# Optimization experiments

Hardware: AMD Instinct MI355X
Metric: run time of the kernel (lower is better)

## Reference

```python
import jax, jax.numpy as jnp
import numpy as np

HIDDEN = 4096
N_HEADS = 32
N_KV_HEADS = 8
HEAD_DIM = 128
ROPE_THETA = 10000.0
B, S = 2, 2048


def _rope_cos_sin(seq_len, head_dim, theta):
    inv_freq = 1.0 / (theta ** (jnp.arange(0, head_dim, 2, dtype=jnp.float32) / head_dim))
    t = jnp.arange(seq_len, dtype=jnp.float32)
    freqs = jnp.einsum('i,j->ij', t, inv_freq)          # [S, D/2]
    emb = jnp.concatenate([freqs, freqs], axis=-1)      # [S, D]
    return jnp.cos(emb), jnp.sin(emb)


def _rotate_half(x):
    x1, x2 = x[..., : x.shape[-1] // 2], x[..., x.shape[-1] // 2 :]
    return jnp.concatenate([-x2, x1], axis=-1)


def setup_inputs() -> dict:
    key = jax.random.key(0)
    k0, k1, k2, k3, k4 = jax.random.split(key, 5)
    scale = 0.02
    return {
        'hidden_states': jax.random.normal(k0, (B, S, HIDDEN), dtype=jnp.float32),
        'wq': jax.random.normal(k1, (N_HEADS * HEAD_DIM, HIDDEN), dtype=jnp.float32) * scale,
        'wk': jax.random.normal(k2, (N_KV_HEADS * HEAD_DIM, HIDDEN), dtype=jnp.float32) * scale,
        'wv': jax.random.normal(k3, (N_KV_HEADS * HEAD_DIM, HIDDEN), dtype=jnp.float32) * scale,
        'wo': jax.random.normal(k4, (HIDDEN, N_HEADS * HEAD_DIM), dtype=jnp.float32) * scale,
    }


def reference(hidden_states, wq, wk, wv, wo):
    bsz, q_len, _ = hidden_states.shape
    n_rep = N_HEADS // N_KV_HEADS

    # Q/K/V projections (nn.Linear: x @ W.T), reshape to [B, H, S, D]
    q = (hidden_states @ wq.T).reshape(bsz, q_len, N_HEADS, HEAD_DIM).transpose(0, 2, 1, 3)
    k = (hidden_states @ wk.T).reshape(bsz, q_len, N_KV_HEADS, HEAD_DIM).transpose(0, 2, 1, 3)
    v = (hidden_states @ wv.T).reshape(bsz, q_len, N_KV_HEADS, HEAD_DIM).transpose(0, 2, 1, 3)

    # RoPE (position_ids = arange) broadcast over heads: cos/sin [1,1,S,D]
    cos, sin = _rope_cos_sin(q_len, HEAD_DIM, ROPE_THETA)
    cos = cos[None, None]
    sin = sin[None, None]
    q = q * cos + _rotate_half(q) * sin
    k = k * cos + _rotate_half(k) * sin

    # repeat_kv: [B, KVH, S, D] -> [B, H, S, D]
    k = jnp.repeat(k, n_rep, axis=1)
    v = jnp.repeat(v, n_rep, axis=1)

    # scaled dot-product attention with causal mask
    scores = jnp.einsum('bhqd,bhkd->bhqk', q, k) / jnp.sqrt(jnp.float32(HEAD_DIM))
    causal = jnp.tril(jnp.ones((q_len, q_len), dtype=bool))
    scores = jnp.where(causal[None, None], scores, jnp.finfo(scores.dtype).min)
    probs = jax.nn.softmax(scores.astype(jnp.float32), axis=-1).astype(q.dtype)
    attn = jnp.einsum('bhqk,bhkd->bhqd', probs, v)

    # merge heads and output projection
    attn = attn.transpose(0, 2, 1, 3).reshape(bsz, q_len, N_HEADS * HEAD_DIM)
    return attn @ wo.T
```

## Files before the change

kernel.cpp:

```cpp
#include <hip/hip_runtime.h>
#include <hip/hip_bf16.h>

typedef __attribute__((ext_vector_type(8))) __bf16 bf16x8;
typedef __attribute__((ext_vector_type(4))) float f32x4;

#define SEQ 2048
#define BATCH 2
#define LDQ 6144

__device__ __forceinline__ void stc(float* p, float v)          { *p = v; }
__device__ __forceinline__ void stc(__hip_bfloat16* p, float v) { *p = __float2bfloat16(v); }

__device__ __forceinline__ void async_copy16(const __hip_bfloat16* g, __hip_bfloat16* lds) {
    __builtin_amdgcn_global_load_lds(
        (const __attribute__((address_space(1))) unsigned int*)g,
        (__attribute__((address_space(3))) unsigned int*)lds,
        16, 0, 0);
}

__global__ void f2b_kernel(const float* __restrict__ s, __hip_bfloat16* __restrict__ d, int n8)
{
    const int i = blockIdx.x * blockDim.x + threadIdx.x;
    if (i >= n8) return;
    const float4 a = ((const float4*)s)[i * 2];
    const float4 b = ((const float4*)s)[i * 2 + 1];
    __hip_bfloat16 t[8];
    t[0] = __float2bfloat16(a.x); t[1] = __float2bfloat16(a.y);
    t[2] = __float2bfloat16(a.z); t[3] = __float2bfloat16(a.w);
    t[4] = __float2bfloat16(b.x); t[5] = __float2bfloat16(b.y);
    t[6] = __float2bfloat16(b.z); t[7] = __float2bfloat16(b.w);
    ((uint4*)d)[i] = *(const uint4*)t;
}

template<typename TC>
__global__ __launch_bounds__(512, 2) void gemm256_kernel(
    const __hip_bfloat16* __restrict__ A,
    const __hip_bfloat16* __restrict__ B,
    TC* __restrict__ C,
    int M, int N, int K)
{
    __shared__ __align__(16) __hip_bfloat16 sAB[2][2][2][256][32];
    const int NT = K >> 6;

    const int tid  = threadIdx.x;
    const int wave = tid >> 6;
    const int lane = tid & 63;
    const int quad = lane >> 4;
    const int l16  = lane & 15;
    const int wm = wave >> 2;
    const int wn = wave & 3;

    const int nbm = M >> 8;
    const int nwg = nbm * (N >> 8);
    int wg = blockIdx.x;
    {
        const int q8 = nwg >> 3, r8 = nwg & 7;
        const int xcd = wg & 7, base = wg >> 3;
        wg = (xcd < r8 ? xcd * (q8 + 1) : r8 * (q8 + 1) + (xcd - r8) * q8) + base;
    }
    const int m0 = (wg % nbm) << 8;
    const int n0 = (wg / nbm) << 8;

    const int srow = lane >> 2;
    const int scol = ((lane & 3) ^ ((lane >> 3) & 3)) * 8;
    const int qsw  = (quad ^ ((l16 >> 1) & 3)) * 8;

    auto stage = [&](int tile, int matr, int kh) {
        const __hip_bfloat16* g = matr ? B : A;
        const int b0 = matr ? n0 : m0;
        const int buf = tile & 1;
        #pragma unroll
        for (int j = 0; j < 2; ++j) {
            const int c = wave * 2 + j;
            async_copy16(g + (size_t)(b0 + c * 16 + srow) * K + tile * 64 + kh * 32 + scol,
                         &sAB[buf][matr][kh][c * 16][0]);
        }
    };

    stage(0, 0, 0); stage(0, 1, 0); stage(0, 0, 1); stage(0, 1, 1);
    stage(1, 0, 0); stage(1, 1, 0);
    asm volatile("s_waitcnt vmcnt(8)" ::: "memory");
    __builtin_amdgcn_s_barrier();

    f32x4 acc[8][4] = {};
    bf16x8 bv[4];

    for (int T = 0; T < NT; ++T) {
        const int buf = T & 1;
        #pragma unroll
        for (int q = 0; q < 4; ++q) {
            const int kh = q >> 1;
            const int rh = (q == 1 || q == 2) ? 1 : 0;

            bf16x8 av[4];
            #pragma unroll
            for (int i = 0; i < 4; ++i)
                av[i] = *(const bf16x8*)&sAB[buf][0][kh][wm * 128 + (rh * 4 + i) * 16 + l16][qsw];
            if (q == 0 || q == 2) {
                #pragma unroll
                for (int j = 0; j < 4; ++j)
                    bv[j] = *(const bf16x8*)&sAB[buf][1][kh][wn * 64 + j * 16 + l16][qsw];
            }

            if (q == 0) { if (T + 1 < NT) stage(T + 1, 0, 1); }
            if (q == 1) { if (T + 1 < NT) stage(T + 1, 1, 1); }
            if (q == 2) { if (T + 2 < NT) stage(T + 2, 0, 0); }
            if (q == 3) { if (T + 2 < NT) stage(T + 2, 1, 0); }

            __builtin_amdgcn_s_barrier();
            asm volatile("s_waitcnt lgkmcnt(0)" ::: "memory");
            __builtin_amdgcn_s_setprio(1);
            #pragma unroll
            for (int i = 0; i < 4; ++i)
                #pragma unroll
                for (int j = 0; j < 4; ++j)
                    acc[rh * 4 + i][j] = __builtin_amdgcn_mfma_f32_16x16x32_bf16(
                        av[i], bv[j], acc[rh * 4 + i][j], 0, 0, 0);
            __builtin_amdgcn_s_setprio(0);

            if (q == 1) {
                if (T < NT - 1)       asm volatile("s_waitcnt vmcnt(8)" ::: "memory");
                else                  asm volatile("s_waitcnt vmcnt(0)" ::: "memory");
            }
            if (q == 3) {
                if (T < NT - 2)       asm volatile("s_waitcnt vmcnt(8)" ::: "memory");
                else if (T == NT - 2) asm volatile("s_waitcnt vmcnt(4)" ::: "memory");
            }
            __builtin_amdgcn_s_barrier();
        }
    }

    #pragma unroll
    for (int i = 0; i < 8; ++i)
        #pragma unroll
        for (int j = 0; j < 4; ++j)
            #pragma unroll
            for (int r = 0; r < 4; ++r) {
                const int m = m0 + wm * 128 + i * 16 + quad * 4 + r;
                const int n = n0 + wn * 64 + j * 16 + l16;
                stc(&C[(size_t)m * N + n], acc[i][j][r]);
            }
}

__global__ void rope_kernel(__hip_bfloat16* __restrict__ X, int rows, int n_heads,
                            int ld, int col0)
{
    const int idx = blockIdx.x * blockDim.x + threadIdx.x;
    const int total = rows * n_heads * 64;
    if (idx >= total) return;
    const int j   = idx & 63;
    const int h   = (idx >> 6) % n_heads;
    const int row = idx / (n_heads * 64);
    const int s   = row & (SEQ - 1);

    const float invf = expf(-(float)j * (9.210340371976184f / 64.0f));
    const float ang = (float)s * invf;
    const float c = cosf(ang), sn = sinf(ang);

    const size_t base = (size_t)row * ld + col0 + h * 128;
    const float x1 = __bfloat162float(X[base + j]);
    const float x2 = __bfloat162float(X[base + 64 + j]);
    X[base + j]      = __float2bfloat16(x1 * c - x2 * sn);
    X[base + 64 + j] = __float2bfloat16(x2 * c + x1 * sn);
}

__global__ __launch_bounds__(256) void vtrans_kernel(
    const __hip_bfloat16* __restrict__ V, __hip_bfloat16* __restrict__ VT)
{
    __shared__ unsigned int T[64][65];

    const int tid = threadIdx.x;
    const int n0 = blockIdx.x * 64;
    const int s0 = blockIdx.y * 64;
    const int b  = blockIdx.z;

    #pragma unroll
    for (int it = 0; it < 2; it++) {
        const int idx = it * 256 + tid;
        const int sr = idx >> 3, nc = (idx & 7) * 8;
        const uint4 v = *(const uint4*)(V + (size_t)(b * SEQ + s0 + sr) * LDQ + n0 + nc);
        const unsigned short* u = (const unsigned short*)&v;
        #pragma unroll
        for (int i = 0; i < 8; i++) T[sr][nc + i] = u[i];
    }
    __syncthreads();
    #pragma unroll
    for (int it = 0; it < 2; it++) {
        const int idx = it * 256 + tid;
        const int nn = idx >> 3, sc = (idx & 7) * 8;
        unsigned short u[8];
        #pragma unroll
        for (int i = 0; i < 8; i++) u[i] = (unsigned short)T[sc + i][nn];
        *(uint4*)(VT + (size_t)(b * 1024 + n0 + nn) * SEQ + s0 + sc) = *(const uint4*)u;
    }
}

__global__ __launch_bounds__(64) void attn_kernel(
    const __hip_bfloat16* __restrict__ QKV,
    const __hip_bfloat16* __restrict__ VT,
    __hip_bfloat16* __restrict__ O)
{
    __shared__ __align__(16) __hip_bfloat16 Pw[2][16][72];

    const int lane = threadIdx.x;
    const int quad = lane >> 4;
    const int l16  = lane & 15;
    const int h   = blockIdx.y;
    const int b   = blockIdx.z;
    const int kvh = h >> 2;

    bf16x8 ones;
    {
        __hip_bfloat16 t[8];
        for (int i = 0; i < 8; i++) t[i] = __float2bfloat16(1.0f);
        ones = *(const bf16x8*)t;
    }

    const __hip_bfloat16* Kbase = QKV + (size_t)b * SEQ * LDQ + 4096 + kvh * 128 + quad * 8;
    const __hip_bfloat16* Vbase = VT + (size_t)(b * 1024 + kvh * 128) * SEQ + quad * 8;
    const float scale = 0.08838834764831845f;
    const float shift = 12.0f;

    for (int ph = 0; ph < 2; ph++) {
        const int qt = ph ? blockIdx.x : 63 - blockIdx.x;
        const int q0 = qt * 32;

        bf16x8 aq[2][4];
        for (int ch = 0; ch < 2; ch++)
            for (int c = 0; c < 4; c++)
                aq[ch][c] = *(const bf16x8*)(QKV + (size_t)(b * SEQ + q0 + ch * 16 + l16) * LDQ
                                                 + h * 128 + c * 32 + quad * 8);

        f32x4 o[2][8] = {};
        f32x4 lsum[2] = {};

        const int nt = qt / 2 + 1;
        for (int kt = 0; kt < nt; kt++) {
            f32x4 sc[2][4] = {};
            #pragma unroll
            for (int g = 0; g < 4; g++) {
                const __hip_bfloat16* kr = Kbase + (size_t)(kt * 64 + g * 16 + l16) * LDQ;
                bf16x8 bk[4];
                #pragma unroll
                for (int c = 0; c < 4; c++) bk[c] = *(const bf16x8*)(kr + c * 32);
                #pragma unroll
                for (int c = 0; c < 4; c++) {
                    sc[0][g] = __builtin_amdgcn_mfma_f32_16x16x32_bf16(aq[0][c], bk[c], sc[0][g], 0, 0, 0);
                    sc[1][g] = __builtin_amdgcn_mfma_f32_16x16x32_bf16(aq[1][c], bk[c], sc[1][g], 0, 0, 0);
                }
            }

            const bool diag = (kt == nt - 1);
            #pragma unroll
            for (int ch = 0; ch < 2; ch++)
                #pragma unroll
                for (int rr = 0; rr < 4; rr++) {
                    float s[4];
                    #pragma unroll
                    for (int g = 0; g < 4; g++) s[g] = sc[ch][g][rr] * scale - shift;
                    if (diag) {
                        const int qg = q0 + ch * 16 + quad * 4 + rr;
                        #pragma unroll
                        for (int g = 0; g < 4; g++)
                            if (kt * 64 + g * 16 + l16 > qg) s[g] = -1e30f;
                    }
                    #pragma unroll
                    for (int g = 0; g < 4; g++)
                        Pw[ch][quad * 4 + rr][g * 16 + l16] = __float2bfloat16(__expf(s[g]));
                }
            asm volatile("s_waitcnt lgkmcnt(0)" ::: "memory");

            bf16x8 ap[2][2];
            #pragma unroll
            for (int ch = 0; ch < 2; ch++) {
                ap[ch][0] = *(const bf16x8*)(&Pw[ch][l16][quad * 8]);
                ap[ch][1] = *(const bf16x8*)(&Pw[ch][l16][32 + quad * 8]);
                lsum[ch] = __builtin_amdgcn_mfma_f32_16x16x32_bf16(ap[ch][0], ones, lsum[ch], 0, 0, 0);
                lsum[ch] = __builtin_amdgcn_mfma_f32_16x16x32_bf16(ap[ch][1], ones, lsum[ch], 0, 0, 0);
            }

            #pragma unroll
            for (int nc = 0; nc < 8; nc++) {
                const __hip_bfloat16* vr = Vbase + (size_t)(nc * 16 + l16) * SEQ + kt * 64;
                const bf16x8 bv0 = *(const bf16x8*)(vr);
                const bf16x8 bv1 = *(const bf16x8*)(vr + 32);
                o[0][nc] = __builtin_amdgcn_mfma_f32_16x16x32_bf16(ap[0][0], bv0, o[0][nc], 0, 0, 0);
                o[0][nc] = __builtin_amdgcn_mfma_f32_16x16x32_bf16(ap[0][1], bv1, o[0][nc], 0, 0, 0);
                o[1][nc] = __builtin_amdgcn_mfma_f32_16x16x32_bf16(ap[1][0], bv0, o[1][nc], 0, 0, 0);
                o[1][nc] = __builtin_amdgcn_mfma_f32_16x16x32_bf16(ap[1][1], bv1, o[1][nc], 0, 0, 0);
            }
        }

        for (int ch = 0; ch < 2; ch++)
            for (int rr = 0; rr < 4; rr++) {
                const float inv = 1.0f / lsum[ch][rr];
                const size_t row = (size_t)(b * SEQ + q0 + ch * 16 + quad * 4 + rr);
                for (int nc = 0; nc < 8; nc++)
                    O[row * 4096 + h * 128 + nc * 16 + l16] = __float2bfloat16(o[ch][nc][rr] * inv);
            }
    }
}

extern "C" void kernel_launch(void* const* d_in, const int* in_sizes, int n_in,
                              void* d_out, int out_size, void* d_ws, size_t ws_size,
                              hipStream_t stream)
{
    const float* X  = (const float*)d_in[0];
    const float* Wq = (const float*)d_in[1];
    const float* Wk = (const float*)d_in[2];
    const float* Wv = (const float*)d_in[3];
    const float* Wo = (const float*)d_in[4];
    float* out = (float*)d_out;

    const size_t MB = 1048576;
    char* ws = (char*)d_ws;
    __hip_bfloat16* Xb   = (__hip_bfloat16*)(ws);
    __hip_bfloat16* WB   = (__hip_bfloat16*)(ws + 32 * MB);
    __hip_bfloat16* Wkb  = (__hip_bfloat16*)(ws + 64 * MB);
    __hip_bfloat16* Wvb  = (__hip_bfloat16*)(ws + 72 * MB);
    __hip_bfloat16* QKVb = (__hip_bfloat16*)(ws + 80 * MB);
    __hip_bfloat16* Ab   = Xb;
    __hip_bfloat16* Wob  = WB;
    __hip_bfloat16* VT   = Wkb;

    const int M = BATCH * SEQ;

    f2b_kernel<<<(M * 4096 / 8 + 255) / 256, 256, 0, stream>>>(X,  Xb,  M * 4096 / 8);
    f2b_kernel<<<(4096 * 4096 / 8 + 255) / 256, 256, 0, stream>>>(Wq, WB,  4096 * 4096 / 8);
    f2b_kernel<<<(1024 * 4096 / 8 + 255) / 256, 256, 0, stream>>>(Wk, Wkb, 1024 * 4096 / 8);
    f2b_kernel<<<(1024 * 4096 / 8 + 255) / 256, 256, 0, stream>>>(Wv, Wvb, 1024 * 4096 / 8);

    gemm256_kernel<__hip_bfloat16>
        <<<dim3((M / 256) * (LDQ / 256)), 512, 0, stream>>>(Xb, WB, QKVb, M, LDQ, 4096);

    f2b_kernel<<<(4096 * 4096 / 8 + 255) / 256, 256, 0, stream>>>(Wo, Wob, 4096 * 4096 / 8);

    rope_kernel<<<(M * 32 * 64 + 255) / 256, 256, 0, stream>>>(QKVb, M, 32, LDQ, 0);
    rope_kernel<<<(M * 8 * 64 + 255) / 256, 256, 0, stream>>>(QKVb, M, 8, LDQ, 4096);

    vtrans_kernel<<<dim3(16, SEQ / 64, BATCH), 256, 0, stream>>>(QKVb + 5120, VT);

    attn_kernel<<<dim3(32, 32, BATCH), 64, 0, stream>>>(QKVb, VT, Ab);

    gemm256_kernel<float>
        <<<dim3((M / 256) * (4096 / 256)), 512, 0, stream>>>(Ab, Wob, out, M, 4096, 4096);
}
```

Baseline: 844.6 us.

## Split attention query tile across two waves per block

The attention kernel now launches 128 threads per block, with each wave handling one 16-row query chunk instead of one wave handling both chunks. This halves per-wave register use for accumulators and doubles the number of waves in flight, to hide global-load latency of K/V. The cost is that each wave loads K and V tiles separately, so global and cache traffic for K/V roughly doubles. No sync is needed because each wave has its own Pw slice.

```diff
diff --git a/kernel.cpp b/kernel.cpp
--- a/kernel.cpp
+++ b/kernel.cpp
@@ -195,14 +195,15 @@
     }
 }
 
-__global__ __launch_bounds__(64) void attn_kernel(
+__global__ __launch_bounds__(128, 4) void attn_kernel(
     const __hip_bfloat16* __restrict__ QKV,
     const __hip_bfloat16* __restrict__ VT,
     __hip_bfloat16* __restrict__ O)
 {
     __shared__ __align__(16) __hip_bfloat16 Pw[2][16][72];
 
-    const int lane = threadIdx.x;
+    const int wv   = threadIdx.x >> 6;
+    const int lane = threadIdx.x & 63;
     const int quad = lane >> 4;
     const int l16  = lane & 15;
     const int h   = blockIdx.y;
@@ -225,18 +226,17 @@
         const int qt = ph ? blockIdx.x : 63 - blockIdx.x;
         const int q0 = qt * 32;
 
-        bf16x8 aq[2][4];
-        for (int ch = 0; ch < 2; ch++)
-            for (int c = 0; c < 4; c++)
-                aq[ch][c] = *(const bf16x8*)(QKV + (size_t)(b * SEQ + q0 + ch * 16 + l16) * LDQ
-                                                 + h * 128 + c * 32 + quad * 8);
-
-        f32x4 o[2][8] = {};
-        f32x4 lsum[2] = {};
+        bf16x8 aq[4];
+        for (int c = 0; c < 4; c++)
+            aq[c] = *(const bf16x8*)(QKV + (size_t)(b * SEQ + q0 + wv * 16 + l16) * LDQ
+                                         + h * 128 + c * 32 + quad * 8);
+
+        f32x4 o[8] = {};
+        f32x4 lsum = {};
 
         const int nt = qt / 2 + 1;
         for (int kt = 0; kt < nt; kt++) {
-            f32x4 sc[2][4] = {};
+            f32x4 sc[4] = {};
             #pragma unroll
             for (int g = 0; g < 4; g++) {
                 const __hip_bfloat16* kr = Kbase + (size_t)(kt * 64 + g * 16 + l16) * LDQ;
@@ -244,60 +244,50 @@
                 #pragma unroll
                 for (int c = 0; c < 4; c++) bk[c] = *(const bf16x8*)(kr + c * 32);
                 #pragma unroll
-                for (int c = 0; c < 4; c++) {
-                    sc[0][g] = __builtin_amdgcn_mfma_f32_16x16x32_bf16(aq[0][c], bk[c], sc[0][g], 0, 0, 0);
-                    sc[1][g] = __builtin_amdgcn_mfma_f32_16x16x32_bf16(aq[1][c], bk[c], sc[1][g], 0, 0, 0);
-                }
+                for (int c = 0; c < 4; c++)
+                    sc[g] = __builtin_amdgcn_mfma_f32_16x16x32_bf16(aq[c], bk[c], sc[g], 0, 0, 0);
             }
 
             const bool diag = (kt == nt - 1);
             #pragma unroll
-            for (int ch = 0; ch < 2; ch++)
-                #pragma unroll
-                for (int rr = 0; rr < 4; rr++) {
-                    float s[4];
-                    #pragma unroll
-                    for (int g = 0; g < 4; g++) s[g] = sc[ch][g][rr] * scale - shift;
-                    if (diag) {
-                        const int qg = q0 + ch * 16 + quad * 4 + rr;
-                        #pragma unroll
-                        for (int g = 0; g < 4; g++)
-                            if (kt * 64 + g * 16 + l16 > qg) s[g] = -1e30f;
-                    }
+            for (int rr = 0; rr < 4; rr++) {
+                float s[4];
+                #pragma unroll
+                for (int g = 0; g < 4; g++) s[g] = sc[g][rr] * scale - shift;
+                if (diag) {
+                    const int qg = q0 + wv * 16 + quad * 4 + rr;
                     #pragma unroll
                     for (int g = 0; g < 4; g++)
-                        Pw[ch][quad * 4 + rr][g * 16 + l16] = __float2bfloat16(__expf(s[g]));
+                        if (kt * 64 + g * 16 + l16 > qg) s[g] = -1e30f;
                 }
+                #pragma unroll
+                for (int g = 0; g < 4; g++)
+                    Pw[wv][quad * 4 + rr][g * 16 + l16] = __float2bfloat16(__expf(s[g]));
+            }
             asm volatile("s_waitcnt lgkmcnt(0)" ::: "memory");
 
-            bf16x8 ap[2][2];
-            #pragma unroll
-            for (int ch = 0; ch < 2; ch++) {
-                ap[ch][0] = *(const bf16x8*)(&Pw[ch][l16][quad * 8]);
-                ap[ch][1] = *(const bf16x8*)(&Pw[ch][l16][32 + quad * 8]);
-                lsum[ch] = __builtin_amdgcn_mfma_f32_16x16x32_bf16(ap[ch][0], ones, lsum[ch], 0, 0, 0);
-                lsum[ch] = __builtin_amdgcn_mfma_f32_16x16x32_bf16(ap[ch][1], ones, lsum[ch], 0, 0, 0);
-            }
+            bf16x8 ap[2];
+            ap[0] = *(const bf16x8*)(&Pw[wv][l16][quad * 8]);
+            ap[1] = *(const bf16x8*)(&Pw[wv][l16][32 + quad * 8]);
+            lsum = __builtin_amdgcn_mfma_f32_16x16x32_bf16(ap[0], ones, lsum, 0, 0, 0);
+            lsum = __builtin_amdgcn_mfma_f32_16x16x32_bf16(ap[1], ones, lsum, 0, 0, 0);
 
             #pragma unroll
             for (int nc = 0; nc < 8; nc++) {
                 const __hip_bfloat16* vr = Vbase + (size_t)(nc * 16 + l16) * SEQ + kt * 64;
                 const bf16x8 bv0 = *(const bf16x8*)(vr);
                 const bf16x8 bv1 = *(const bf16x8*)(vr + 32);
-                o[0][nc] = __builtin_amdgcn_mfma_f32_16x16x32_bf16(ap[0][0], bv0, o[0][nc], 0, 0, 0);
-                o[0][nc] = __builtin_amdgcn_mfma_f32_16x16x32_bf16(ap[0][1], bv1, o[0][nc], 0, 0, 0);
-                o[1][nc] = __builtin_amdgcn_mfma_f32_16x16x32_bf16(ap[1][0], bv0, o[1][nc], 0, 0, 0);
-                o[1][nc] = __builtin_amdgcn_mfma_f32_16x16x32_bf16(ap[1][1], bv1, o[1][nc], 0, 0, 0);
+                o[nc] = __builtin_amdgcn_mfma_f32_16x16x32_bf16(ap[0], bv0, o[nc], 0, 0, 0);
+                o[nc] = __builtin_amdgcn_mfma_f32_16x16x32_bf16(ap[1], bv1, o[nc], 0, 0, 0);
             }
         }
 
-        for (int ch = 0; ch < 2; ch++)
-            for (int rr = 0; rr < 4; rr++) {
-                const float inv = 1.0f / lsum[ch][rr];
-                const size_t row = (size_t)(b * SEQ + q0 + ch * 16 + quad * 4 + rr);
-                for (int nc = 0; nc < 8; nc++)
-                    O[row * 4096 + h * 128 + nc * 16 + l16] = __float2bfloat16(o[ch][nc][rr] * inv);
-            }
+        for (int rr = 0; rr < 4; rr++) {
+            const float inv = 1.0f / lsum[rr];
+            const size_t row = (size_t)(b * SEQ + q0 + wv * 16 + quad * 4 + rr);
+            for (int nc = 0; nc < 8; nc++)
+                O[row * 4096 + h * 128 + nc * 16 + l16] = __float2bfloat16(o[nc][rr] * inv);
+        }
     }
 }
 
@@ -340,7 +330,7 @@
 
     vtrans_kernel<<<dim3(16, SEQ / 64, BATCH), 256, 0, stream>>>(QKVb + 5120, VT);
 
-    attn_kernel<<<dim3(32, 32, BATCH), 64, 0, stream>>>(QKVb, VT, Ab);
+    attn_kernel<<<dim3(32, 32, BATCH), 128, 0, stream>>>(QKVb, VT, Ab);
 
     gemm256_kernel<float>
         <<<dim3((M / 256) * (4096 / 256)), 512, 0, stream>>>(Ab, Wob, out, M, 4096, 4096);
```

Measured after the change: 1.068 ms. 26.4% more time.
